# Performance work log

Hardware: AMD Instinct MI355X
Metric: run time of the kernel (lower is better)

## Reference

```python
import jax, jax.numpy as jnp
import numpy as np

BITS = 4
N_PACK = 32 // BITS  # int32 compression
GROUPSIZE = 128
MASK = (1 << BITS) - 1


def _unpack_int32(q, axis):
    """Unpack int32 tensor into N_PACK low-bit values along `axis`.
    Element j*N_PACK+e comes from bits [BITS*e, BITS*(e+1)) of packed word j."""
    parts = [ (q >> (BITS * e)) & MASK for e in range(N_PACK) ]
    u = jnp.stack(parts, axis=axis + 1)  # (..., P, N_PACK, ...)
    shape = list(q.shape)
    shape[axis] = shape[axis] * N_PACK
    return u.reshape(shape)


def setup_inputs() -> dict:
    key = jax.random.key(0)
    k1, k2, k3, k4, k5 = jax.random.split(key, 5)
    in_f, out_f = 4096, 12288
    tokens = 8192
    n_groups = in_f // GROUPSIZE  # 32
    x = jax.random.normal(k1, (tokens, in_f), dtype=jnp.float32)
    scales = jax.random.uniform(k2, (n_groups, out_f), dtype=jnp.float32) * 0.01 + 1e-3
    bias = jax.random.normal(k3, (out_f,), dtype=jnp.float32)
    qweight = jax.random.randint(k4, (in_f // N_PACK, out_f), jnp.iinfo(jnp.int32).min, jnp.iinfo(jnp.int32).max, dtype=jnp.int32)
    qzeros = jax.random.randint(k5, (n_groups, out_f // N_PACK), jnp.iinfo(jnp.int32).min, jnp.iinfo(jnp.int32).max, dtype=jnp.int32)
    return {"x": x, "scales": scales, "bias": bias, "qweight": qweight, "qzeros": qzeros}


def reference(x, scales, bias, qweight, qzeros):
    in_f = qweight.shape[0] * N_PACK
    out_f = qweight.shape[1]
    n_groups = scales.shape[0]
    # Unpack 4-bit weights along input-channel axis: (in_f, out_f), values 0..15
    w_int = _unpack_int32(qweight, axis=0).astype(scales.dtype)
    # Unpack zero points along output-channel axis; optimum format stores zp-1
    zp = (_unpack_int32(qzeros, axis=1) + 1).astype(scales.dtype)  # (n_groups, out_f)
    # Per-group dequant: group g covers input channels [g*GROUPSIZE, (g+1)*GROUPSIZE)
    w = (w_int.reshape(n_groups, GROUPSIZE, out_f) - zp[:, None, :]) * scales[:, None, :]
    w = w.reshape(in_f, out_f)
    # Linear: y = x @ W^T with W = w.T, i.e. x @ w
    return x @ w + bias
```

## Files before the change

### kernel.cpp

```cpp
#include <hip/hip_runtime.h>
#include <hip/hip_bf16.h>


typedef __attribute__((ext_vector_type(8))) short short8;
typedef __attribute__((ext_vector_type(4))) float f32x4;

__device__ __forceinline__ short f2bf(float f) {
  unsigned u = __float_as_uint(f);
  u += 0x7fffu + ((u >> 16) & 1u);
  return (short)(u >> 16);
}

__device__ __forceinline__ void gload_lds16(const void* g, void* l) {
  __builtin_amdgcn_global_load_lds(
      (const __attribute__((address_space(1))) void*)g,
      (__attribute__((address_space(3))) void*)l,
      16, 0, 0);
}

__device__ __forceinline__ void bar() {
  asm volatile("" ::: "memory");
  __builtin_amdgcn_s_barrier();
  asm volatile("" ::: "memory");
}
__device__ __forceinline__ void wait_vm8() {
  asm volatile("s_waitcnt vmcnt(8)" ::: "memory");
}
__device__ __forceinline__ void wait_vm0() {
  asm volatile("s_waitcnt vmcnt(0)" ::: "memory");
}

__global__ __launch_bounds__(256) void dequant_kernel(
    const int* __restrict__ qweight, const int* __restrict__ qzeros,
    const float* __restrict__ scales, short* __restrict__ Wt,
    int in_f, int out_f) {
  __shared__ __align__(16) short T[64][72];
  const int n0 = blockIdx.x * 64;
  const int k0 = blockIdx.y * 64;
  const int t = threadIdx.x;
  const int nl = t & 63;
  const int kw = t >> 6;
  const int n = n0 + nl;
  const int g = k0 >> 7;
  const float sc = scales[(size_t)g * out_f + n];
  const int zpw = qzeros[(size_t)g * (out_f >> 3) + (n >> 3)];
  const float zp = (float)(((zpw >> ((n & 7) * 4)) & 15) + 1);
  const float zs = zp * sc;
#pragma unroll
  for (int rr = 0; rr < 2; ++rr) {
    const int kwi = kw + rr * 4;
    const int w = qweight[(size_t)((k0 >> 3) + kwi) * out_f + n];
    short8 v;
#pragma unroll
    for (int e = 0; e < 8; ++e) {
      float f = (float)((w >> (4 * e)) & 15) * sc - zs;
      v[e] = f2bf(f);
    }
    *(short8*)&T[nl][kwi * 8] = v;
  }
  __syncthreads();
#pragma unroll
  for (int rr = 0; rr < 2; ++rr) {
    const int c = rr * 256 + t;
    const int row = c >> 3, ch = c & 7;
    *(short8*)&Wt[(size_t)(n0 + row) * in_f + k0 + ch * 8] =
        *(const short8*)&T[row][ch * 8];
  }
}

__global__ __launch_bounds__(256) void cvt_kernel(
    const float* __restrict__ x, short* __restrict__ xb, long n8) {
  long i = (long)blockIdx.x * blockDim.x + threadIdx.x;
  if (i >= n8) return;
  const float* src = x + i * 8;
  float4 a = *(const float4*)src;
  float4 b = *(const float4*)(src + 4);
  short8 v;
  v[0] = f2bf(a.x); v[1] = f2bf(a.y); v[2] = f2bf(a.z); v[3] = f2bf(a.w);
  v[4] = f2bf(b.x); v[5] = f2bf(b.y); v[6] = f2bf(b.z); v[7] = f2bf(b.w);
  *(short8*)(xb + i * 8) = v;
}

#define GBM 256
#define GBN 256
#define GBK 64

__global__ __launch_bounds__(512, 2) void gemm256_kernel(
    const short* __restrict__ A, const short* __restrict__ Bt,
    const float* __restrict__ bias, float* __restrict__ C,
    int M, int N, int K) {
  __shared__ __align__(16) short lds[2][2][GBM * GBK];
  const int tid = threadIdx.x;
  const int nbx = N / GBN;
  const int nwg = gridDim.x;
  int bid = blockIdx.x;
  if ((nwg & 7) == 0) bid = (bid & 7) * (nwg >> 3) + (bid >> 3);
  const int bm = (bid / nbx) * GBM;
  const int bn = (bid % nbx) * GBN;

  const int wid = tid >> 6, lane = tid & 63;
  const int wr = wid >> 2, wc = wid & 3;
  const int lrow = lane & 15;
  const int lkq = lane >> 4;

  const int NT = K / GBK;

  auto STAGE = [&](int b, int kt) {
#pragma unroll
    for (int r = 0; r < 4; ++r) {
      const int c = r * 512 + tid;
      const int row = c >> 3;
      const int ch = (c & 7) ^ (row & 7);
      gload_lds16(A + (size_t)(bm + row) * K + kt + ch * 8,
                  (char*)&lds[b][0][0] + c * 16);
    }
#pragma unroll
    for (int r = 0; r < 4; ++r) {
      const int c = r * 512 + tid;
      const int row = c >> 3;
      const int ch = (c & 7) ^ (row & 7);
      gload_lds16(Bt + (size_t)(bn + row) * K + kt + ch * 8,
                  (char*)&lds[b][1][0] + c * 16);
    }
  };

  f32x4 acc[8][4] = {};

  STAGE(0, 0);
  if (NT > 1) { STAGE(1, GBK); wait_vm8(); } else { wait_vm0(); }
  bar();

  int cur = 0;
  for (int t = 0; t < NT; ++t) {
    const char* Ab = (const char*)&lds[cur][0][0];
    const char* Bb = (const char*)&lds[cur][1][0];
    short8 bfr[4], afr[4];
#pragma unroll
    for (int kk = 0; kk < 2; ++kk) {
#pragma unroll
      for (int mh = 0; mh < 2; ++mh) {
        if (mh == 0) {
#pragma unroll
          for (int j = 0; j < 4; ++j) {
            const int row = wc * 64 + j * 16 + lrow;
            const int q = (kk * 4 + lkq) ^ (row & 7);
            bfr[j] = *(const short8*)(Bb + row * 128 + q * 16);
          }
        }
#pragma unroll
        for (int i = 0; i < 4; ++i) {
          const int row = wr * 128 + (mh * 4 + i) * 16 + lrow;
          const int q = (kk * 4 + lkq) ^ (row & 7);
          afr[i] = *(const short8*)(Ab + row * 128 + q * 16);
        }
        bar();
        __builtin_amdgcn_s_setprio(1);
#pragma unroll
        for (int i = 0; i < 4; ++i)
#pragma unroll
          for (int j = 0; j < 4; ++j)
            acc[mh * 4 + i][j] = __builtin_amdgcn_mfma_f32_16x16x32_bf16(
                afr[i], bfr[j], acc[mh * 4 + i][j], 0, 0, 0);
        __builtin_amdgcn_s_setprio(0);
        bar();
      }
    }
    if (t == NT - 1) break;
    if (t + 2 < NT) {
      STAGE(cur, (t + 2) * GBK);
      wait_vm8();
    } else {
      wait_vm0();
    }
    bar();
    cur ^= 1;
  }

  const int crow0 = bm + wr * 128 + (lane >> 4) * 4;
  const int ccol0 = bn + wc * 64 + (lane & 15);
#pragma unroll
  for (int j = 0; j < 4; ++j) {
    const float bv = bias[ccol0 + j * 16];
#pragma unroll
    for (int i = 0; i < 8; ++i) {
#pragma unroll
      for (int r = 0; r < 4; ++r) {
        C[(size_t)(crow0 + i * 16 + r) * N + ccol0 + j * 16] =
            acc[i][j][r] + bv;
      }
    }
  }
}

#define BM 128
#define BN 128
#define BK 64

template <bool A_BF16>
__global__ __launch_bounds__(256) void gemm_bias_kernel(
    const void* __restrict__ Av, const short* __restrict__ Bt,
    const float* __restrict__ bias, float* __restrict__ C,
    int M, int N, int K) {
  __shared__ __align__(16) short As[BM * BK];
  __shared__ __align__(16) short Bs[BN * BK];
  const int tid = threadIdx.x;
  const int bm = blockIdx.y * BM;
  const int bn = blockIdx.x * BN;
  const int wid = tid >> 6, lane = tid & 63;
  const int wr = wid >> 1, wc = wid & 1;
  const int lrow = lane & 15;
  const int lk = (lane >> 4) * 8;

  f32x4 acc[4][4] = {};

  for (int kt = 0; kt < K; kt += BK) {
    if constexpr (A_BF16) {
      const short* A = (const short*)Av;
#pragma unroll
      for (int r = 0; r < 4; ++r) {
        const int c = r * 256 + tid;
        const int row = c >> 3, ch = c & 7;
        gload_lds16(A + (size_t)(bm + row) * K + kt + ch * 8,
                    (char*)As + c * 16);
      }
    } else {
      const float* A = (const float*)Av;
#pragma unroll
      for (int r = 0; r < 4; ++r) {
        const int c = r * 256 + tid;
        const int row = c >> 3, ch = c & 7;
        const float* src = A + (size_t)(bm + row) * K + kt + ch * 8;
        float4 f0 = *(const float4*)src;
        float4 f1 = *(const float4*)(src + 4);
        short8 v;
        v[0] = f2bf(f0.x); v[1] = f2bf(f0.y); v[2] = f2bf(f0.z); v[3] = f2bf(f0.w);
        v[4] = f2bf(f1.x); v[5] = f2bf(f1.y); v[6] = f2bf(f1.z); v[7] = f2bf(f1.w);
        *(short8*)((char*)As + c * 16) = v;
      }
    }
#pragma unroll
    for (int r = 0; r < 4; ++r) {
      const int c = r * 256 + tid;
      const int row = c >> 3, ch = c & 7;
      gload_lds16(Bt + (size_t)(bn + row) * K + kt + ch * 8,
                  (char*)Bs + c * 16);
    }
    __syncthreads();
#pragma unroll
    for (int kk = 0; kk < 2; ++kk) {
      short8 af[4], bf[4];
#pragma unroll
      for (int i = 0; i < 4; ++i)
        af[i] = *(const short8*)&As[(wr * 64 + i * 16 + lrow) * BK + kk * 32 + lk];
#pragma unroll
      for (int j = 0; j < 4; ++j)
        bf[j] = *(const short8*)&Bs[(wc * 64 + j * 16 + lrow) * BK + kk * 32 + lk];
#pragma unroll
      for (int i = 0; i < 4; ++i)
#pragma unroll
        for (int j = 0; j < 4; ++j)
          acc[i][j] = __builtin_amdgcn_mfma_f32_16x16x32_bf16(
              af[i], bf[j], acc[i][j], 0, 0, 0);
    }
    __syncthreads();
  }

  const int crow0 = bm + wr * 64 + (lane >> 4) * 4;
  const int ccol0 = bn + wc * 64 + (lane & 15);
#pragma unroll
  for (int j = 0; j < 4; ++j) {
    const float bv = bias[ccol0 + j * 16];
#pragma unroll
    for (int i = 0; i < 4; ++i) {
#pragma unroll
      for (int r = 0; r < 4; ++r) {
        C[(size_t)(crow0 + i * 16 + r) * N + ccol0 + j * 16] = acc[i][j][r] + bv;
      }
    }
  }
}

__global__ __launch_bounds__(256) void naive_kernel(
    const float* __restrict__ x, const float* __restrict__ scales,
    const float* __restrict__ bias, const int* __restrict__ qw,
    const int* __restrict__ qz, float* __restrict__ out,
    int M, int K, int N) {
  long idx = (long)blockIdx.x * blockDim.x + threadIdx.x;
  if (idx >= (long)M * N) return;
  const int n = (int)(idx % N);
  const int m = (int)(idx / N);
  float acc = 0.f;
  for (int g = 0; g < K / 128; ++g) {
    const float sc = scales[(size_t)g * N + n];
    const float zp =
        (float)(((qz[(size_t)g * (N >> 3) + (n >> 3)] >> ((n & 7) * 4)) & 15) + 1);
    const float zs = zp * sc;
    for (int kw = 0; kw < 16; ++kw) {
      const int w = qw[(size_t)(g * 16 + kw) * N + n];
      const float* xp = &x[(size_t)m * K + g * 128 + kw * 8];
#pragma unroll
      for (int e = 0; e < 8; ++e)
        acc += xp[e] * ((float)((w >> (4 * e)) & 15) * sc - zs);
    }
  }
  out[idx] = acc + bias[n];
}

extern "C" void kernel_launch(void* const* d_in, const int* in_sizes, int n_in,
                              void* d_out, int out_size, void* d_ws,
                              size_t ws_size, hipStream_t stream) {
  const float* x = (const float*)d_in[0];
  const float* scales = (const float*)d_in[1];
  const float* bias = (const float*)d_in[2];
  const int* qweight = (const int*)d_in[3];
  const int* qzeros = (const int*)d_in[4];
  float* out = (float*)d_out;

  const int out_f = in_sizes[2];
  const int kwords = in_sizes[3] / out_f;
  const int in_f = kwords * 8;
  const int tokens = in_sizes[0] / in_f;
  const int M = tokens, K = in_f, N = out_f;

  const size_t wt_bytes = (size_t)K * N * sizeof(short);
  const size_t xb_bytes = (size_t)M * K * sizeof(short);

  const bool div128 = (M % BM == 0) && (N % BN == 0) && (K % BK == 0) &&
                      (K % 128 == 0) && (N % 64 == 0);
  const bool div256 = (M % GBM == 0) && (N % GBN == 0) && (K % GBK == 0) &&
                      (K % 128 == 0) && (N % 64 == 0);

  if (div128 && ws_size >= wt_bytes + xb_bytes) {
    short* Wt = (short*)d_ws;
    short* xb = (short*)((char*)d_ws + wt_bytes);
    dequant_kernel<<<dim3(N / 64, K / 64), 256, 0, stream>>>(
        qweight, qzeros, scales, Wt, K, N);
    const long n8 = (long)M * K / 8;
    cvt_kernel<<<(int)((n8 + 255) / 256), 256, 0, stream>>>(x, xb, n8);
    if (div256) {
      gemm256_kernel<<<(M / GBM) * (N / GBN), 512, 0, stream>>>(
          xb, Wt, bias, out, M, N, K);
    } else {
      gemm_bias_kernel<true><<<dim3(N / BN, M / BM), 256, 0, stream>>>(
          xb, Wt, bias, out, M, N, K);
    }
  } else if (div128 && ws_size >= wt_bytes) {
    short* Wt = (short*)d_ws;
    dequant_kernel<<<dim3(N / 64, K / 64), 256, 0, stream>>>(
        qweight, qzeros, scales, Wt, K, N);
    gemm_bias_kernel<false><<<dim3(N / BN, M / BM), 256, 0, stream>>>(
        x, Wt, bias, out, M, N, K);
  } else {
    const long total = (long)M * N;
    naive_kernel<<<(int)((total + 255) / 256), 256, 0, stream>>>(
        x, scales, bias, qweight, qzeros, out, M, K, N);
  }
}
```

Measured before the change: 926.0 us.

## Interleave staged global-to-LDS loads with MFMA quadrants in 8-phase GEMM loop

Restructures the 256x256 GEMM main loop into an unrolled two-tile, eight-phase schedule. Each phase reads a sub-block of A/B fragments, issues a quarter of the next tile's global-to-LDS loads, synchronizes, then runs a 4x2 quadrant of MFMAs. The goal is to spread memory traffic evenly across compute and tighten vmcnt waits so load latency stays hidden. It adds more barriers per tile, and it assumes an even number of K tiles, which the relaxed divisibility check (K%128) is meant to guarantee.

After: 976.7 us. 5.5% more time.

```diff
diff --git a/kernel.cpp b/kernel.cpp
--- a/kernel.cpp
+++ b/kernel.cpp
@@ -23,11 +23,17 @@
   __builtin_amdgcn_s_barrier();
   asm volatile("" ::: "memory");
 }
-__device__ __forceinline__ void wait_vm8() {
-  asm volatile("s_waitcnt vmcnt(8)" ::: "memory");
+__device__ __forceinline__ void wait_vm2() {
+  asm volatile("s_waitcnt vmcnt(2)" ::: "memory");
 }
 __device__ __forceinline__ void wait_vm0() {
   asm volatile("s_waitcnt vmcnt(0)" ::: "memory");
+}
+__device__ __forceinline__ void phase_sync() {
+  asm volatile("" ::: "memory");
+  __builtin_amdgcn_s_barrier();
+  asm volatile("s_waitcnt lgkmcnt(0)" ::: "memory");
+  __builtin_amdgcn_sched_barrier(0);
 }
 
 __global__ __launch_bounds__(256) void dequant_kernel(
@@ -105,18 +111,20 @@
 
   const int NT = K / GBK;
 
-  auto STAGE = [&](int b, int kt) {
-#pragma unroll
-    for (int r = 0; r < 4; ++r) {
-      const int c = r * 512 + tid;
+  auto stA = [&](int b, int kt, int r0) {
+#pragma unroll
+    for (int r = 0; r < 2; ++r) {
+      const int c = (r0 + r) * 512 + tid;
       const int row = c >> 3;
       const int ch = (c & 7) ^ (row & 7);
       gload_lds16(A + (size_t)(bm + row) * K + kt + ch * 8,
                   (char*)&lds[b][0][0] + c * 16);
     }
-#pragma unroll
-    for (int r = 0; r < 4; ++r) {
-      const int c = r * 512 + tid;
+  };
+  auto stB = [&](int b, int kt, int r0) {
+#pragma unroll
+    for (int r = 0; r < 2; ++r) {
+      const int c = (r0 + r) * 512 + tid;
       const int row = c >> 3;
       const int ch = (c & 7) ^ (row & 7);
       gload_lds16(Bt + (size_t)(bn + row) * K + kt + ch * 8,
@@ -124,56 +132,77 @@
     }
   };
 
+  short8 af[4][2], bf[4][2];
   f32x4 acc[8][4] = {};
 
-  STAGE(0, 0);
-  if (NT > 1) { STAGE(1, GBK); wait_vm8(); } else { wait_vm0(); }
+  auto rdA = [&](const char* base, int ih) {
+#pragma unroll
+    for (int i = 0; i < 4; ++i) {
+      const int row = wr * 128 + ih * 64 + i * 16 + lrow;
+#pragma unroll
+      for (int kk = 0; kk < 2; ++kk) {
+        const int q = (kk * 4 + lkq) ^ (row & 7);
+        af[i][kk] = *(const short8*)(base + row * 128 + q * 16);
+      }
+    }
+  };
+  auto rdB = [&](const char* base, int jh) {
+#pragma unroll
+    for (int j = 0; j < 2; ++j) {
+      const int row = wc * 64 + (jh * 2 + j) * 16 + lrow;
+#pragma unroll
+      for (int kk = 0; kk < 2; ++kk) {
+        const int q = (kk * 4 + lkq) ^ (row & 7);
+        bf[jh * 2 + j][kk] = *(const short8*)(base + row * 128 + q * 16);
+      }
+    }
+  };
+  auto quad = [&](int ib, int jb) {
+    __builtin_amdgcn_s_setprio(1);
+#pragma unroll
+    for (int kk = 0; kk < 2; ++kk)
+#pragma unroll
+      for (int i = 0; i < 4; ++i)
+#pragma unroll
+        for (int j = 0; j < 2; ++j)
+          acc[ib + i][jb + j] = __builtin_amdgcn_mfma_f32_16x16x32_bf16(
+              af[i][kk], bf[jb + j][kk], acc[ib + i][jb + j], 0, 0, 0);
+    __builtin_amdgcn_s_setprio(0);
+  };
+
+  const char* A0 = (const char*)&lds[0][0][0];
+  const char* B0 = (const char*)&lds[0][1][0];
+  const char* A1 = (const char*)&lds[1][0][0];
+  const char* B1 = (const char*)&lds[1][1][0];
+
+  stA(0, 0, 0); stA(0, 0, 2); stB(0, 0, 0); stB(0, 0, 2);
+  if (NT > 1) { stA(1, GBK, 0); wait_vm2(); } else { wait_vm0(); }
   bar();
 
-  int cur = 0;
-  for (int t = 0; t < NT; ++t) {
-    const char* Ab = (const char*)&lds[cur][0][0];
-    const char* Bb = (const char*)&lds[cur][1][0];
-    short8 bfr[4], afr[4];
-#pragma unroll
-    for (int kk = 0; kk < 2; ++kk) {
-#pragma unroll
-      for (int mh = 0; mh < 2; ++mh) {
-        if (mh == 0) {
-#pragma unroll
-          for (int j = 0; j < 4; ++j) {
-            const int row = wc * 64 + j * 16 + lrow;
-            const int q = (kk * 4 + lkq) ^ (row & 7);
-            bfr[j] = *(const short8*)(Bb + row * 128 + q * 16);
-          }
-        }
-#pragma unroll
-        for (int i = 0; i < 4; ++i) {
-          const int row = wr * 128 + (mh * 4 + i) * 16 + lrow;
-          const int q = (kk * 4 + lkq) ^ (row & 7);
-          afr[i] = *(const short8*)(Ab + row * 128 + q * 16);
-        }
-        bar();
-        __builtin_amdgcn_s_setprio(1);
-#pragma unroll
-        for (int i = 0; i < 4; ++i)
-#pragma unroll
-          for (int j = 0; j < 4; ++j)
-            acc[mh * 4 + i][j] = __builtin_amdgcn_mfma_f32_16x16x32_bf16(
-                afr[i], bfr[j], acc[mh * 4 + i][j], 0, 0, 0);
-        __builtin_amdgcn_s_setprio(0);
-        bar();
-      }
-    }
-    if (t == NT - 1) break;
-    if (t + 2 < NT) {
-      STAGE(cur, (t + 2) * GBK);
-      wait_vm8();
-    } else {
-      wait_vm0();
-    }
-    bar();
-    cur ^= 1;
+  for (int t = 0; t < NT; t += 2) {
+    const bool more = (t + 2 < NT);
+    rdA(A0, 0); rdB(B0, 0);
+    stA(1, (t + 1) * GBK, 2);
+    phase_sync(); quad(0, 0); bar();
+    rdB(B0, 1);
+    stB(1, (t + 1) * GBK, 0);
+    phase_sync(); quad(0, 2); bar();
+    rdA(A0, 1);
+    stB(1, (t + 1) * GBK, 2);
+    phase_sync(); quad(4, 0); bar();
+    if (more) { stA(0, (t + 2) * GBK, 0); wait_vm2(); } else { wait_vm0(); }
+    phase_sync(); quad(4, 2); bar();
+    rdA(A1, 0); rdB(B1, 0);
+    if (more) stA(0, (t + 2) * GBK, 2);
+    phase_sync(); quad(0, 0); bar();
+    rdB(B1, 1);
+    if (more) stB(0, (t + 2) * GBK, 0);
+    phase_sync(); quad(0, 2); bar();
+    rdA(A1, 1);
+    if (more) stB(0, (t + 2) * GBK, 2);
+    phase_sync(); quad(4, 0); bar();
+    if (more) { stA(1, (t + 3) * GBK, 0); wait_vm2(); }
+    phase_sync(); quad(4, 2); bar();
   }
 
   const int crow0 = bm + wr * 128 + (lane >> 4) * 4;
@@ -327,8 +356,8 @@
 
   const bool div128 = (M % BM == 0) && (N % BN == 0) && (K % BK == 0) &&
                       (K % 128 == 0) && (N % 64 == 0);
-  const bool div256 = (M % GBM == 0) && (N % GBN == 0) && (K % GBK == 0) &&
-                      (K % 128 == 0) && (N % 64 == 0);
+  const bool div256 = (M % GBM == 0) && (N % GBN == 0) && (K % 128 == 0) &&
+                      (N % 64 == 0);
 
   if (div128 && ws_size >= wt_bytes + xb_bytes) {
     short* Wt = (short*)d_ws;
```

## Restructure GEMM into 4-stage BK=32 LDS ring with one barrier per phase

Applied to the files above, without the earlier changes.

Replaces the double-buffered BK=64 main loop with a four-slot ring of BK=32 stages. Each phase prefetches three stages ahead, waits with a vmcnt count, and issues one barrier instead of several. LDS offsets and swizzle are precomputed once and use a smaller 64-byte row stride with a new XOR pattern. The aim is to hide global-to-LDS latency and cut barrier overhead. The cost is smaller K chunks per barrier and a deeper pipeline, which may need careful vmcnt accounting.

After: 847.9 us. 8.4% less time.

```diff
diff --git a/kernel.cpp b/kernel.cpp
--- a/kernel.cpp
+++ b/kernel.cpp
@@ -25,6 +25,9 @@
 }
 __device__ __forceinline__ void wait_vm8() {
   asm volatile("s_waitcnt vmcnt(8)" ::: "memory");
+}
+__device__ __forceinline__ void wait_vm4() {
+  asm volatile("s_waitcnt vmcnt(4)" ::: "memory");
 }
 __device__ __forceinline__ void wait_vm0() {
   asm volatile("s_waitcnt vmcnt(0)" ::: "memory");
@@ -83,13 +86,12 @@
 
 #define GBM 256
 #define GBN 256
-#define GBK 64
 
 __global__ __launch_bounds__(512, 2) void gemm256_kernel(
     const short* __restrict__ A, const short* __restrict__ Bt,
     const float* __restrict__ bias, float* __restrict__ C,
     int M, int N, int K) {
-  __shared__ __align__(16) short lds[2][2][GBM * GBK];
+  __shared__ __align__(16) char lds[4][32768];
   const int tid = threadIdx.x;
   const int nbx = N / GBN;
   const int nwg = gridDim.x;
@@ -101,80 +103,88 @@
   const int wid = tid >> 6, lane = tid & 63;
   const int wr = wid >> 2, wc = wid & 3;
   const int lrow = lane & 15;
-  const int lkq = lane >> 4;
-
-  const int NT = K / GBK;
-
-  auto STAGE = [&](int b, int kt) {
-#pragma unroll
-    for (int r = 0; r < 4; ++r) {
-      const int c = r * 512 + tid;
-      const int row = c >> 3;
-      const int ch = (c & 7) ^ (row & 7);
-      gload_lds16(A + (size_t)(bm + row) * K + kt + ch * 8,
-                  (char*)&lds[b][0][0] + c * 16);
-    }
-#pragma unroll
-    for (int r = 0; r < 4; ++r) {
-      const int c = r * 512 + tid;
-      const int row = c >> 3;
-      const int ch = (c & 7) ^ (row & 7);
-      gload_lds16(Bt + (size_t)(bn + row) * K + kt + ch * 8,
-                  (char*)&lds[b][1][0] + c * 16);
-    }
+  const int lq = lane >> 4;
+
+  const int P = K >> 5;
+
+  int offA[2][4], offB[4];
+#pragma unroll
+  for (int mh = 0; mh < 2; ++mh)
+#pragma unroll
+    for (int i = 0; i < 4; ++i) {
+      const int row = wr * 128 + mh * 64 + i * 16 + lrow;
+      const int s = lq ^ ((row >> 1) & 3);
+      offA[mh][i] = row * 64 + s * 16;
+    }
+#pragma unroll
+  for (int j = 0; j < 4; ++j) {
+    const int row = wc * 64 + j * 16 + lrow;
+    const int s = lq ^ ((row >> 1) & 3);
+    offB[j] = 16384 + row * 64 + s * 16;
+  }
+
+  const int c0 = tid, c1 = tid + 512;
+  const int rA0 = c0 >> 2, qA0 = (c0 & 3) ^ ((rA0 >> 1) & 3);
+  const int rA1 = c1 >> 2, qA1 = (c1 & 3) ^ ((rA1 >> 1) & 3);
+  const short* srcA0 = A + (size_t)(bm + rA0) * K + qA0 * 8;
+  const short* srcA1 = A + (size_t)(bm + rA1) * K + qA1 * 8;
+  const short* srcB0 = Bt + (size_t)(bn + rA0) * K + qA0 * 8;
+  const short* srcB1 = Bt + (size_t)(bn + rA1) * K + qA1 * 8;
+  const int dA0 = c0 * 16, dA1 = c1 * 16;
+  const int dB0 = 16384 + c0 * 16, dB1 = 16384 + c1 * 16;
+
+  auto STAGE = [&](int slot, int h) {
+    const int kof = h * 32;
+    char* sb = &lds[slot][0];
+    gload_lds16(srcA0 + kof, sb + dA0);
+    gload_lds16(srcA1 + kof, sb + dA1);
+    gload_lds16(srcB0 + kof, sb + dB0);
+    gload_lds16(srcB1 + kof, sb + dB1);
   };
 
   f32x4 acc[8][4] = {};
 
+  auto PHASE = [&](int p, bool doStage) {
+    const char* sb = &lds[p & 3][0];
+    short8 bf[4], af[4];
+#pragma unroll
+    for (int j = 0; j < 4; ++j) bf[j] = *(const short8*)(sb + offB[j]);
+#pragma unroll
+    for (int i = 0; i < 4; ++i) af[i] = *(const short8*)(sb + offA[0][i]);
+    if (doStage) STAGE((p + 3) & 3, p + 3);
+    __builtin_amdgcn_s_setprio(1);
+#pragma unroll
+    for (int i = 0; i < 4; ++i)
+#pragma unroll
+      for (int j = 0; j < 4; ++j)
+        acc[i][j] = __builtin_amdgcn_mfma_f32_16x16x32_bf16(
+            af[i], bf[j], acc[i][j], 0, 0, 0);
+    __builtin_amdgcn_s_setprio(0);
+    short8 af2[4];
+#pragma unroll
+    for (int i = 0; i < 4; ++i) af2[i] = *(const short8*)(sb + offA[1][i]);
+    __builtin_amdgcn_s_setprio(1);
+#pragma unroll
+    for (int i = 0; i < 4; ++i)
+#pragma unroll
+      for (int j = 0; j < 4; ++j)
+        acc[4 + i][j] = __builtin_amdgcn_mfma_f32_16x16x32_bf16(
+            af2[i], bf[j], acc[4 + i][j], 0, 0, 0);
+    __builtin_amdgcn_s_setprio(0);
+  };
+
   STAGE(0, 0);
-  if (NT > 1) { STAGE(1, GBK); wait_vm8(); } else { wait_vm0(); }
-  bar();
-
-  int cur = 0;
-  for (int t = 0; t < NT; ++t) {
-    const char* Ab = (const char*)&lds[cur][0][0];
-    const char* Bb = (const char*)&lds[cur][1][0];
-    short8 bfr[4], afr[4];
-#pragma unroll
-    for (int kk = 0; kk < 2; ++kk) {
-#pragma unroll
-      for (int mh = 0; mh < 2; ++mh) {
-        if (mh == 0) {
-#pragma unroll
-          for (int j = 0; j < 4; ++j) {
-            const int row = wc * 64 + j * 16 + lrow;
-            const int q = (kk * 4 + lkq) ^ (row & 7);
-            bfr[j] = *(const short8*)(Bb + row * 128 + q * 16);
-          }
-        }
-#pragma unroll
-        for (int i = 0; i < 4; ++i) {
-          const int row = wr * 128 + (mh * 4 + i) * 16 + lrow;
-          const int q = (kk * 4 + lkq) ^ (row & 7);
-          afr[i] = *(const short8*)(Ab + row * 128 + q * 16);
-        }
-        bar();
-        __builtin_amdgcn_s_setprio(1);
-#pragma unroll
-        for (int i = 0; i < 4; ++i)
-#pragma unroll
-          for (int j = 0; j < 4; ++j)
-            acc[mh * 4 + i][j] = __builtin_amdgcn_mfma_f32_16x16x32_bf16(
-                afr[i], bfr[j], acc[mh * 4 + i][j], 0, 0, 0);
-        __builtin_amdgcn_s_setprio(0);
-        bar();
-      }
-    }
-    if (t == NT - 1) break;
-    if (t + 2 < NT) {
-      STAGE(cur, (t + 2) * GBK);
-      wait_vm8();
-    } else {
-      wait_vm0();
-    }
+  STAGE(1, 1);
+  STAGE(2, 2);
+
+  for (int p = 0; p <= P - 4; ++p) {
+    wait_vm8();
     bar();
-    cur ^= 1;
-  }
+    PHASE(p, true);
+  }
+  wait_vm8(); bar(); PHASE(P - 3, false);
+  wait_vm4(); bar(); PHASE(P - 2, false);
+  wait_vm0(); bar(); PHASE(P - 1, false);
 
   const int crow0 = bm + wr * 128 + (lane >> 4) * 4;
   const int ccol0 = bn + wc * 64 + (lane & 15);
@@ -327,8 +337,8 @@
 
   const bool div128 = (M % BM == 0) && (N % BN == 0) && (K % BK == 0) &&
                       (K % 128 == 0) && (N % 64 == 0);
-  const bool div256 = (M % GBM == 0) && (N % GBN == 0) && (K % GBK == 0) &&
-                      (K % 128 == 0) && (N % 64 == 0);
+  const bool div256 = (M % GBM == 0) && (N % GBN == 0) && (K % 128 == 0) &&
+                      (N % 64 == 0);
 
   if (div128 && ws_size >= wt_bytes + xb_bytes) {
     short* Wt = (short*)d_ws;
```
